# Kernel tuning notes

Hardware: AMD Instinct MI355X
Metric: run time of the kernel (lower is better)

The kernel has to match this reference:

```python
import jax, jax.numpy as jnp
import numpy as np

B, S, N, D = 8, 4096, 1024, 1024
NUM_WIDTH, WIDTH_DIM, MAX_WIDTH = 64, 64, 32


def setup_inputs() -> dict:
    key = jax.random.key(0)
    k_seq, k_start, k_width, k_w, k_emb = jax.random.split(key, 5)
    sequence_tensor = jax.random.normal(k_seq, (B, S, D), dtype=jnp.float32)
    starts = jax.random.randint(k_start, (B, N), 0, S)
    widths = jax.random.randint(k_width, (B, N), 0, MAX_WIDTH)
    ends = jnp.minimum(starts + widths, S - 1)
    span_indices = jnp.stack([starts, ends], axis=-1).astype(jnp.int64)
    att_weight = jax.random.normal(k_w, (1, D), dtype=jnp.float32) * 0.02
    att_bias = jnp.zeros((1,), dtype=jnp.float32)
    width_embedding = jax.random.normal(k_emb, (NUM_WIDTH, WIDTH_DIM), dtype=jnp.float32) * 0.02
    return {
        "sequence_tensor": sequence_tensor,
        "span_indices": span_indices,
        "att_weight": att_weight,
        "att_bias": att_bias,
        "width_embedding": width_embedding,
    }


def _span_attend(sequence_tensor, span_indices, att_weight, att_bias):
    # per-token attention logit: (B, S)
    logits = jnp.einsum("bsd,d->bs", sequence_tensor, att_weight[0]) + att_bias[0]
    starts = span_indices[..., 0]  # (B, N)
    ends = span_indices[..., 1]    # (B, N)
    valid = (starts >= 0) & (ends >= starts)  # (B, N)
    pos = jnp.arange(sequence_tensor.shape[1])  # (S,)
    # membership mask: (B, N, S)
    in_span = (pos[None, None, :] >= starts[..., None]) & (pos[None, None, :] <= ends[..., None])
    neg_inf = jnp.asarray(-jnp.inf, logits.dtype)
    scores = jnp.where(in_span, logits[:, None, :], neg_inf)  # (B, N, S)
    # stable masked softmax; fully-masked rows yield all-zero weights
    m = jnp.max(scores, axis=-1, keepdims=True)
    m = jnp.where(jnp.isfinite(m), m, 0.0)
    e = jnp.exp(scores - m)
    denom = jnp.sum(e, axis=-1, keepdims=True)
    attn = e / jnp.where(denom > 0, denom, 1.0)  # (B, N, S)
    span_emb = jnp.einsum("bns,bsd->bnd", attn, sequence_tensor)  # (B, N, D)
    span_emb = jnp.where(valid[..., None], span_emb, 0.0)
    return span_emb, starts, ends


def reference(sequence_tensor, span_indices, att_weight, att_bias, width_embedding):
    span_emb, starts, ends = _span_attend(sequence_tensor, span_indices, att_weight, att_bias)
    widths = jnp.clip(ends - starts, 0, NUM_WIDTH - 1)  # (B, N)
    width_emb = width_embedding[widths]  # (B, N, WIDTH_DIM)
    return jnp.concatenate([span_emb, width_emb], axis=-1)
```

## Files before the change

kernel.cpp:

```cpp
#include <hip/hip_runtime.h>

#define BB 8
#define SS 4096
#define NN 1024
#define DD 1024
#define NUM_WIDTH 64
#define WIDTH_DIM 64
#define OUTD (DD + WIDTH_DIM)
#define NSPAN (BB * NN)
#define NBUCK 128
#define NBINS (BB * NBUCK)

__global__ __launch_bounds__(1024) void sort_kernel(const int* __restrict__ idx,
                                                    int* __restrict__ perm) {
    __shared__ int lds[NBINS];
    int tid = threadIdx.x;
    lds[tid] = 0;
    __syncthreads();

    for (int i = tid; i < NSPAN; i += 1024) {
        int start = idx[i * 2];
        int b = i >> 10;
        int s0 = start > 0 ? start : 0;
        if (s0 > SS - 1) s0 = SS - 1;
        atomicAdd(&lds[b * NBUCK + (s0 >> 5)], 1);
    }
    __syncthreads();

    for (int off = 1; off < NBINS; off <<= 1) {
        int add = (tid >= off) ? lds[tid - off] : 0;
        __syncthreads();
        lds[tid] += add;
        __syncthreads();
    }
    int ex = (tid > 0) ? lds[tid - 1] : 0;
    __syncthreads();
    lds[tid] = ex;
    __syncthreads();

    for (int i = tid; i < NSPAN; i += 1024) {
        int start = idx[i * 2];
        int b = i >> 10;
        int s0 = start > 0 ? start : 0;
        if (s0 > SS - 1) s0 = SS - 1;
        int pos = atomicAdd(&lds[b * NBUCK + (s0 >> 5)], 1);
        perm[pos] = i;
    }
}

__global__ __launch_bounds__(256) void span_kernel(const float* __restrict__ seq,
                                                   const int* __restrict__ idx,
                                                   const float* __restrict__ w,
                                                   const float* __restrict__ wemb,
                                                   const int* __restrict__ perm,
                                                   float* __restrict__ out) {
    int swz = (blockIdx.x & 7) * (NSPAN / 8) + (blockIdx.x >> 3);
    int bn  = perm[swz];
    int b   = bn >> 10;
    int tid = threadIdx.x;
    int wave = tid >> 6;
    int lane = tid & 63;

    int start = idx[bn * 2 + 0];
    int end   = idx[bn * 2 + 1];
    int s0 = start > 0 ? start : 0;
    int e0 = end < (SS - 1) ? end : (SS - 1);
    int L  = (start >= 0 && end >= start) ? (e0 - s0 + 1) : 0;
    if (L < 0) L = 0;
    if (L > 32) L = 32;

    if (tid < WIDTH_DIM) {
        int wdt = end - start;
        if (wdt < 0) wdt = 0;
        if (wdt > NUM_WIDTH - 1) wdt = NUM_WIDTH - 1;
        out[(long long)bn * OUTD + DD + tid] = wemb[wdt * WIDTH_DIM + tid];
    }

    __shared__ float lds_acc[4][DD];
    __shared__ float lds_m[4], lds_z[4];

    const float4* s4 = (const float4*)(seq + ((long long)b * SS + s0) * DD);
    const float4* w4 = (const float4*)w;
    float4 wr0 = w4[lane], wr1 = w4[64 + lane], wr2 = w4[128 + lane], wr3 = w4[192 + lane];

    float m = -INFINITY, Z = 0.f;
    float4 acc0 = make_float4(0.f, 0.f, 0.f, 0.f);
    float4 acc1 = acc0, acc2 = acc0, acc3 = acc0;

    for (int r = wave; r < L; r += 4) {
        const float4* row = s4 + (long long)r * (DD / 4);
        float4 a0 = row[lane], a1 = row[64 + lane], a2 = row[128 + lane], a3 = row[192 + lane];
        float dot = a0.x * wr0.x + a0.y * wr0.y + a0.z * wr0.z + a0.w * wr0.w
                  + a1.x * wr1.x + a1.y * wr1.y + a1.z * wr1.z + a1.w * wr1.w
                  + a2.x * wr2.x + a2.y * wr2.y + a2.z * wr2.z + a2.w * wr2.w
                  + a3.x * wr3.x + a3.y * wr3.y + a3.z * wr3.z + a3.w * wr3.w;
        #pragma unroll
        for (int d = 32; d >= 1; d >>= 1)
            dot += __shfl_xor(dot, d, 64);
        if (dot > m) {
            float f = __expf(m - dot);
            Z *= f;
            acc0.x *= f; acc0.y *= f; acc0.z *= f; acc0.w *= f;
            acc1.x *= f; acc1.y *= f; acc1.z *= f; acc1.w *= f;
            acc2.x *= f; acc2.y *= f; acc2.z *= f; acc2.w *= f;
            acc3.x *= f; acc3.y *= f; acc3.z *= f; acc3.w *= f;
            m = dot;
        }
        float e = __expf(dot - m);
        Z += e;
        acc0.x += e * a0.x; acc0.y += e * a0.y; acc0.z += e * a0.z; acc0.w += e * a0.w;
        acc1.x += e * a1.x; acc1.y += e * a1.y; acc1.z += e * a1.z; acc1.w += e * a1.w;
        acc2.x += e * a2.x; acc2.y += e * a2.y; acc2.z += e * a2.z; acc2.w += e * a2.w;
        acc3.x += e * a3.x; acc3.y += e * a3.y; acc3.z += e * a3.z; acc3.w += e * a3.w;
    }

    if (lane == 0) { lds_m[wave] = m; lds_z[wave] = Z; }
    float4* la = (float4*)lds_acc[wave];
    la[lane] = acc0; la[64 + lane] = acc1; la[128 + lane] = acc2; la[192 + lane] = acc3;
    __syncthreads();

    float m0 = lds_m[0], m1 = lds_m[1], m2 = lds_m[2], m3 = lds_m[3];
    float mg = fmaxf(fmaxf(m0, m1), fmaxf(m2, m3));
    float f0 = (m0 == -INFINITY) ? 0.f : __expf(m0 - mg);
    float f1 = (m1 == -INFINITY) ? 0.f : __expf(m1 - mg);
    float f2 = (m2 == -INFINITY) ? 0.f : __expf(m2 - mg);
    float f3 = (m3 == -INFINITY) ? 0.f : __expf(m3 - mg);
    float Zg = f0 * lds_z[0] + f1 * lds_z[1] + f2 * lds_z[2] + f3 * lds_z[3];
    float inv = (Zg > 0.f) ? 1.0f / Zg : 0.f;

    float4 r0 = ((float4*)lds_acc[0])[tid];
    float4 r1 = ((float4*)lds_acc[1])[tid];
    float4 r2 = ((float4*)lds_acc[2])[tid];
    float4 r3 = ((float4*)lds_acc[3])[tid];
    float4 o;
    o.x = (f0 * r0.x + f1 * r1.x + f2 * r2.x + f3 * r3.x) * inv;
    o.y = (f0 * r0.y + f1 * r1.y + f2 * r2.y + f3 * r3.y) * inv;
    o.z = (f0 * r0.z + f1 * r1.z + f2 * r2.z + f3 * r3.z) * inv;
    o.w = (f0 * r0.w + f1 * r1.w + f2 * r2.w + f3 * r3.w) * inv;

    float4* o4 = (float4*)(out + (long long)bn * OUTD);
    o4[tid] = o;
}

extern "C" void kernel_launch(void* const* d_in, const int* in_sizes, int n_in,
                              void* d_out, int out_size, void* d_ws, size_t ws_size,
                              hipStream_t stream) {
    const float* seq  = (const float*)d_in[0];
    const int*   idx  = (const int*)d_in[1];
    const float* w    = (const float*)d_in[2];
    const float* wemb = (const float*)d_in[4];
    float* out = (float*)d_out;

    int* perm = (int*)d_ws;

    sort_kernel<<<1, 1024, 0, stream>>>(idx, perm);
    span_kernel<<<NSPAN, 256, 0, stream>>>(seq, idx, w, wemb, perm, out);
}
```

Measured before the change: 47.28 us.

## Unroll span rows by two, pack span metadata, and use wave-shuffle scan in sort

The span kernel now processes two rows per wave per iteration, issuing both rows' loads before reducing, so memory-level parallelism rises and fewer serial shuffle/rescale steps run per row. The sort kernel replaces the LDS Hillis-Steele scan with a wave-shuffle scan. It also writes an int4 record holding the index, start and end, so the span kernel avoids a dependent reload of the span indices. The cost is more registers per thread and a tail path for odd row counts.

After: 49.29 us. 4.2% more time.

```diff
diff --git a/kernel.cpp b/kernel.cpp
--- a/kernel.cpp
+++ b/kernel.cpp
@@ -11,58 +11,68 @@
 #define NBUCK 128
 #define NBINS (BB * NBUCK)
 
-__global__ __launch_bounds__(1024) void sort_kernel(const int* __restrict__ idx,
-                                                    int* __restrict__ perm) {
-    __shared__ int lds[NBINS];
-    int tid = threadIdx.x;
-    lds[tid] = 0;
+__global__ __launch_bounds__(1024) void sort_kernel(const int2* __restrict__ idx2,
+                                                    int4* __restrict__ meta) {
+    __shared__ int cnt[NBINS];
+    __shared__ int wsum[16];
+    int tid = threadIdx.x, lane = tid & 63, wid = tid >> 6;
+    cnt[tid] = 0;
     __syncthreads();
 
     for (int i = tid; i < NSPAN; i += 1024) {
-        int start = idx[i * 2];
-        int b = i >> 10;
-        int s0 = start > 0 ? start : 0;
+        int2 se = idx2[i];
+        int s0 = se.x > 0 ? se.x : 0;
         if (s0 > SS - 1) s0 = SS - 1;
-        atomicAdd(&lds[b * NBUCK + (s0 >> 5)], 1);
-    }
-    __syncthreads();
-
-    for (int off = 1; off < NBINS; off <<= 1) {
-        int add = (tid >= off) ? lds[tid - off] : 0;
-        __syncthreads();
-        lds[tid] += add;
-        __syncthreads();
-    }
-    int ex = (tid > 0) ? lds[tid - 1] : 0;
-    __syncthreads();
-    lds[tid] = ex;
+        atomicAdd(&cnt[(i >> 10) * NBUCK + (s0 >> 5)], 1);
+    }
+    __syncthreads();
+
+    int orig = cnt[tid];
+    int x = orig;
+    #pragma unroll
+    for (int d = 1; d < 64; d <<= 1) {
+        int y = __shfl_up(x, d, 64);
+        if (lane >= d) x += y;
+    }
+    if (lane == 63) wsum[wid] = x;
+    __syncthreads();
+    if (wid == 0) {
+        int s = (lane < 16) ? wsum[lane] : 0;
+        #pragma unroll
+        for (int d = 1; d < 16; d <<= 1) {
+            int y = __shfl_up(s, d, 64);
+            if (lane >= d) s += y;
+        }
+        if (lane < 16) wsum[lane] = s;
+    }
+    __syncthreads();
+    int excl = x - orig + (wid > 0 ? wsum[wid - 1] : 0);
+    __syncthreads();
+    cnt[tid] = excl;
     __syncthreads();
 
     for (int i = tid; i < NSPAN; i += 1024) {
-        int start = idx[i * 2];
-        int b = i >> 10;
-        int s0 = start > 0 ? start : 0;
+        int2 se = idx2[i];
+        int s0 = se.x > 0 ? se.x : 0;
         if (s0 > SS - 1) s0 = SS - 1;
-        int pos = atomicAdd(&lds[b * NBUCK + (s0 >> 5)], 1);
-        perm[pos] = i;
+        int pos = atomicAdd(&cnt[(i >> 10) * NBUCK + (s0 >> 5)], 1);
+        meta[pos] = make_int4(i, se.x, se.y, 0);
     }
 }
 
 __global__ __launch_bounds__(256) void span_kernel(const float* __restrict__ seq,
-                                                   const int* __restrict__ idx,
                                                    const float* __restrict__ w,
                                                    const float* __restrict__ wemb,
-                                                   const int* __restrict__ perm,
+                                                   const int4* __restrict__ meta,
                                                    float* __restrict__ out) {
     int swz = (blockIdx.x & 7) * (NSPAN / 8) + (blockIdx.x >> 3);
-    int bn  = perm[swz];
-    int b   = bn >> 10;
+    int4 me = meta[swz];
+    int bn = me.x, start = me.y, end = me.z;
+    int b  = bn >> 10;
     int tid = threadIdx.x;
     int wave = tid >> 6;
     int lane = tid & 63;
 
-    int start = idx[bn * 2 + 0];
-    int end   = idx[bn * 2 + 1];
     int s0 = start > 0 ? start : 0;
     int e0 = end < (SS - 1) ? end : (SS - 1);
     int L  = (start >= 0 && end >= start) ? (e0 - s0 + 1) : 0;
@@ -87,31 +97,72 @@
     float4 acc0 = make_float4(0.f, 0.f, 0.f, 0.f);
     float4 acc1 = acc0, acc2 = acc0, acc3 = acc0;
 
-    for (int r = wave; r < L; r += 4) {
-        const float4* row = s4 + (long long)r * (DD / 4);
-        float4 a0 = row[lane], a1 = row[64 + lane], a2 = row[128 + lane], a3 = row[192 + lane];
-        float dot = a0.x * wr0.x + a0.y * wr0.y + a0.z * wr0.z + a0.w * wr0.w
-                  + a1.x * wr1.x + a1.y * wr1.y + a1.z * wr1.z + a1.w * wr1.w
-                  + a2.x * wr2.x + a2.y * wr2.y + a2.z * wr2.z + a2.w * wr2.w
-                  + a3.x * wr3.x + a3.y * wr3.y + a3.z * wr3.z + a3.w * wr3.w;
+    int r = wave;
+    for (; r + 4 < L; r += 8) {
+        const float4* rowA = s4 + (long long)r * (DD / 4);
+        const float4* rowB = rowA + DD;
+        float4 a0 = rowA[lane], a1 = rowA[64 + lane], a2 = rowA[128 + lane], a3 = rowA[192 + lane];
+        float4 b0 = rowB[lane], b1 = rowB[64 + lane], b2 = rowB[128 + lane], b3 = rowB[192 + lane];
+        float dA = a0.x * wr0.x + a0.y * wr0.y + a0.z * wr0.z + a0.w * wr0.w
+                 + a1.x * wr1.x + a1.y * wr1.y + a1.z * wr1.z + a1.w * wr1.w
+                 + a2.x * wr2.x + a2.y * wr2.y + a2.z * wr2.z + a2.w * wr2.w
+                 + a3.x * wr3.x + a3.y * wr3.y + a3.z * wr3.z + a3.w * wr3.w;
+        float dB = b0.x * wr0.x + b0.y * wr0.y + b0.z * wr0.z + b0.w * wr0.w
+                 + b1.x * wr1.x + b1.y * wr1.y + b1.z * wr1.z + b1.w * wr1.w
+                 + b2.x * wr2.x + b2.y * wr2.y + b2.z * wr2.z + b2.w * wr2.w
+                 + b3.x * wr3.x + b3.y * wr3.y + b3.z * wr3.z + b3.w * wr3.w;
         #pragma unroll
-        for (int d = 32; d >= 1; d >>= 1)
-            dot += __shfl_xor(dot, d, 64);
-        if (dot > m) {
-            float f = __expf(m - dot);
+        for (int d = 32; d >= 1; d >>= 1) {
+            dA += __shfl_xor(dA, d, 64);
+            dB += __shfl_xor(dB, d, 64);
+        }
+        float dm = fmaxf(dA, dB);
+        if (dm > m) {
+            float f = __expf(m - dm);
             Z *= f;
             acc0.x *= f; acc0.y *= f; acc0.z *= f; acc0.w *= f;
             acc1.x *= f; acc1.y *= f; acc1.z *= f; acc1.w *= f;
             acc2.x *= f; acc2.y *= f; acc2.z *= f; acc2.w *= f;
             acc3.x *= f; acc3.y *= f; acc3.z *= f; acc3.w *= f;
-            m = dot;
-        }
-        float e = __expf(dot - m);
-        Z += e;
-        acc0.x += e * a0.x; acc0.y += e * a0.y; acc0.z += e * a0.z; acc0.w += e * a0.w;
-        acc1.x += e * a1.x; acc1.y += e * a1.y; acc1.z += e * a1.z; acc1.w += e * a1.w;
-        acc2.x += e * a2.x; acc2.y += e * a2.y; acc2.z += e * a2.z; acc2.w += e * a2.w;
-        acc3.x += e * a3.x; acc3.y += e * a3.y; acc3.z += e * a3.z; acc3.w += e * a3.w;
+            m = dm;
+        }
+        float eA = __expf(dA - m);
+        float eB = __expf(dB - m);
+        Z += eA + eB;
+        acc0.x += eA * a0.x + eB * b0.x; acc0.y += eA * a0.y + eB * b0.y;
+        acc0.z += eA * a0.z + eB * b0.z; acc0.w += eA * a0.w + eB * b0.w;
+        acc1.x += eA * a1.x + eB * b1.x; acc1.y += eA * a1.y + eB * b1.y;
+        acc1.z += eA * a1.z + eB * b1.z; acc1.w += eA * a1.w + eB * b1.w;
+        acc2.x += eA * a2.x + eB * b2.x; acc2.y += eA * a2.y + eB * b2.y;
+        acc2.z += eA * a2.z + eB * b2.z; acc2.w += eA * a2.w + eB * b2.w;
+        acc3.x += eA * a3.x + eB * b3.x; acc3.y += eA * a3.y + eB * b3.y;
+        acc3.z += eA * a3.z + eB * b3.z; acc3.w += eA * a3.w + eB * b3.w;
+    }
+    if (r < L) {
+        const float4* rowA = s4 + (long long)r * (DD / 4);
+        float4 a0 = rowA[lane], a1 = rowA[64 + lane], a2 = rowA[128 + lane], a3 = rowA[192 + lane];
+        float dA = a0.x * wr0.x + a0.y * wr0.y + a0.z * wr0.z + a0.w * wr0.w
+                 + a1.x * wr1.x + a1.y * wr1.y + a1.z * wr1.z + a1.w * wr1.w
+                 + a2.x * wr2.x + a2.y * wr2.y + a2.z * wr2.z + a2.w * wr2.w
+                 + a3.x * wr3.x + a3.y * wr3.y + a3.z * wr3.z + a3.w * wr3.w;
+        #pragma unroll
+        for (int d = 32; d >= 1; d >>= 1)
+            dA += __shfl_xor(dA, d, 64);
+        if (dA > m) {
+            float f = __expf(m - dA);
+            Z *= f;
+            acc0.x *= f; acc0.y *= f; acc0.z *= f; acc0.w *= f;
+            acc1.x *= f; acc1.y *= f; acc1.z *= f; acc1.w *= f;
+            acc2.x *= f; acc2.y *= f; acc2.z *= f; acc2.w *= f;
+            acc3.x *= f; acc3.y *= f; acc3.z *= f; acc3.w *= f;
+            m = dA;
+        }
+        float eA = __expf(dA - m);
+        Z += eA;
+        acc0.x += eA * a0.x; acc0.y += eA * a0.y; acc0.z += eA * a0.z; acc0.w += eA * a0.w;
+        acc1.x += eA * a1.x; acc1.y += eA * a1.y; acc1.z += eA * a1.z; acc1.w += eA * a1.w;
+        acc2.x += eA * a2.x; acc2.y += eA * a2.y; acc2.z += eA * a2.z; acc2.w += eA * a2.w;
+        acc3.x += eA * a3.x; acc3.y += eA * a3.y; acc3.z += eA * a3.z; acc3.w += eA * a3.w;
     }
 
     if (lane == 0) { lds_m[wave] = m; lds_z[wave] = Z; }
@@ -151,8 +202,8 @@
     const float* wemb = (const float*)d_in[4];
     float* out = (float*)d_out;
 
-    int* perm = (int*)d_ws;
-
-    sort_kernel<<<1, 1024, 0, stream>>>(idx, perm);
-    span_kernel<<<NSPAN, 256, 0, stream>>>(seq, idx, w, wemb, perm, out);
+    int4* meta = (int4*)d_ws;
+
+    sort_kernel<<<1, 1024, 0, stream>>>((const int2*)idx, meta);
+    span_kernel<<<NSPAN, 256, 0, stream>>>(seq, w, wemb, meta, out);
 }
```
